# Performance work log

Hardware: AMD Instinct MI355X
Metric: run time of the kernel (lower is better)

## Reference

```python
import jax, jax.numpy as jnp
import numpy as np

EMB_DIM = 2048
N_Q_HEADS = 32
N_KV_HEADS = 8
HEAD_DIM = EMB_DIM // N_Q_HEADS  # 64
N_REP = N_Q_HEADS // N_KV_HEADS  # 4
ROPE_BASE = 10000.0


def setup_inputs() -> dict:
    key = jax.random.key(0)
    ks = jax.random.split(key, 9)
    B, T = 2, 2048
    kv_dim = HEAD_DIM * N_KV_HEADS
    s = 0.02
    return {
        "x":  jax.random.normal(ks[0], (B, T, EMB_DIM), jnp.float32),
        "Wq": jax.random.normal(ks[1], (EMB_DIM, EMB_DIM), jnp.float32) * s,
        "bq": jax.random.normal(ks[2], (EMB_DIM,), jnp.float32) * s,
        "Wk": jax.random.normal(ks[3], (kv_dim, EMB_DIM), jnp.float32) * s,
        "bk": jax.random.normal(ks[4], (kv_dim,), jnp.float32) * s,
        "Wv": jax.random.normal(ks[5], (kv_dim, EMB_DIM), jnp.float32) * s,
        "bv": jax.random.normal(ks[6], (kv_dim,), jnp.float32) * s,
        "Wo": jax.random.normal(ks[7], (EMB_DIM, EMB_DIM), jnp.float32) * s,
        "bo": jax.random.normal(ks[8], (EMB_DIM,), jnp.float32) * s,
    }


def _rope_tables(T, D, dtype):
    inv_freq = 1.0 / (ROPE_BASE ** (jnp.arange(0, D, 2, dtype=jnp.float32) / D))
    t = jnp.arange(T, dtype=jnp.float32)
    freqs = jnp.einsum("i,j->ij", t, inv_freq)          # [T, D/2]
    emb = jnp.concatenate([freqs, freqs], axis=-1)       # [T, D]
    # broadcast over batch and heads: [1, T, 1, D]
    return jnp.cos(emb)[None, :, None, :].astype(dtype), jnp.sin(emb)[None, :, None, :].astype(dtype)


def _rotate_half(x):
    x1, x2 = jnp.split(x, 2, axis=-1)
    return jnp.concatenate([-x2, x1], axis=-1)


def reference(x, Wq, bq, Wk, bk, Wv, bv, Wo, bo):
    B, T, C = x.shape
    q = (x @ Wq.T + bq).reshape(B, T, N_Q_HEADS, HEAD_DIM)
    k = (x @ Wk.T + bk).reshape(B, T, N_KV_HEADS, HEAD_DIM)
    v = (x @ Wv.T + bv).reshape(B, T, N_KV_HEADS, HEAD_DIM)

    cos, sin = _rope_tables(T, HEAD_DIM, x.dtype)
    q = q * cos + _rotate_half(q) * sin
    k = k * cos + _rotate_half(k) * sin

    q = q.transpose(0, 2, 1, 3)                          # [B, Hq, T, D]
    k = k.transpose(0, 2, 1, 3)                          # [B, Hkv, T, D]
    v = v.transpose(0, 2, 1, 3)
    # GQA: repeat_interleave kv heads to match query heads
    k = jnp.repeat(k, N_REP, axis=1)                     # [B, Hq, T, D]
    v = jnp.repeat(v, N_REP, axis=1)

    scale = 1.0 / jnp.sqrt(jnp.asarray(HEAD_DIM, x.dtype))
    att = jnp.einsum("bhqd,bhkd->bhqk", q, k) * scale    # [B, Hq, T, T]
    causal = jnp.tril(jnp.ones((T, T), dtype=bool))
    att = jnp.where(causal[None, None], att, -jnp.inf)
    att = jax.nn.softmax(att, axis=-1)

    y = jnp.einsum("bhqk,bhkd->bhqd", att, v)            # [B, Hq, T, D]
    y = y.transpose(0, 2, 1, 3).reshape(B, T, C)
    return y @ Wo.T + bo
```

## Files before the change

kernel.cpp:

```cpp
#include <hip/hip_runtime.h>
#include <hip/hip_bf16.h>
#include <math.h>


typedef __attribute__((ext_vector_type(8))) short short8;
typedef __attribute__((ext_vector_type(4))) float f32x4;
typedef __attribute__((ext_vector_type(16))) float f32x16;
typedef __attribute__((ext_vector_type(2))) unsigned int uint2v;

#define MFMA16(a,b,c) __builtin_amdgcn_mfma_f32_16x16x32_bf16((a),(b),(c),0,0,0)
#define MFMA32(a,b,c) __builtin_amdgcn_mfma_f32_32x32x16_bf16((a),(b),(c),0,0,0)
#define QSCALE 0.18033688011112043f
#define NFREQ  (-13.28771237954945f / 32.0f)

__device__ __forceinline__ ushort f2bf(float f) {
  union { float f; unsigned u; } x; x.f = f;
  unsigned r = x.u + 0x7fffu + ((x.u >> 16) & 1u);
  return (ushort)(r >> 16);
}
__device__ __forceinline__ uint pkbf(float a, float b) {
  union { float f; unsigned u; } x, y; x.f = a; y.f = b;
  return ((x.u + 0x8000u) >> 16) | ((y.u + 0x8000u) & 0xffff0000u);
}

__device__ __forceinline__ void g2l16(const void* g, void* l) {
  __builtin_amdgcn_global_load_lds(
      (__attribute__((address_space(1))) void*)g,
      (__attribute__((address_space(3))) void*)l, 16, 0, 0);
}

__global__ void cvt_all(const float* __restrict__ x,  const float* __restrict__ wq,
                        const float* __restrict__ wk, const float* __restrict__ wv,
                        const float* __restrict__ wo,
                        ushort* __restrict__ x_bf, ushort* __restrict__ wqkv,
                        ushort* __restrict__ wo_bf) {
  int i = blockIdx.x * 256 + threadIdx.x;
  const float4* src; ushort* dst; int off;
  if (i < 2097152)      { src = (const float4*)x;  dst = x_bf;             off = i; }
  else if (i < 3145728) { src = (const float4*)wq; dst = wqkv;             off = i - 2097152; }
  else if (i < 3407872) { src = (const float4*)wk; dst = wqkv + 4194304;   off = i - 3145728; }
  else if (i < 3670016) { src = (const float4*)wv; dst = wqkv + 5242880;   off = i - 3407872; }
  else                  { src = (const float4*)wo; dst = wo_bf;            off = i - 3670016; }
  float4 v = src[off];
  ushort4 o;
  o.x = f2bf(v.x); o.y = f2bf(v.y); o.z = f2bf(v.z); o.w = f2bf(v.w);
  ((ushort4*)dst)[off] = o;
}

__global__ __launch_bounds__(256, 3)
void gemm_qkv(const ushort* __restrict__ A, const ushort* __restrict__ Bw,
              const float* __restrict__ bq, const float* __restrict__ bk,
              const float* __restrict__ bv,
              ushort* __restrict__ qr, ushort* __restrict__ kr,
              ushort* __restrict__ vt) {
  const int K = 2048;
  __shared__ ushort As[2][128*32];
  __shared__ ushort Bs[2][128*32];
  const int tid = threadIdx.x;
  const int wave = tid >> 6, lane = tid & 63;
  const int wm = wave >> 1, wn = wave & 1;
  const int quad = lane >> 4, l16 = lane & 15;
  const int swg = (l16 >> 1) & 3;
  int id = blockIdx.y * 24 + blockIdx.x;
  id = (id & 7) * 96 + (id >> 3);
  const int bx = id % 24, by = id / 24;
  const int m0 = by * 128, n0 = bx * 128;

  f32x4 acc[4][4] = {};

  auto stage = [&](int buf, int k0) {
#pragma unroll
    for (int i = 0; i < 2; ++i) {
      int cbase = (i*4 + wave) * 64;
      int p = cbase + lane;
      int row = p >> 2, pcb = p & 3;
      int cl = pcb ^ ((row >> 1) & 3);
      g2l16(A  + (size_t)(m0 + row) * K + k0 + cl * 8, As[buf] + (size_t)cbase * 8);
      g2l16(Bw + (size_t)(n0 + row) * K + k0 + cl * 8, Bs[buf] + (size_t)cbase * 8);
    }
  };

  stage(0, 0);
  for (int k0 = 0; k0 < K; k0 += 32) {
    __syncthreads();
    int cur = (k0 >> 5) & 1;
    if (k0 + 32 < K) stage(cur ^ 1, k0 + 32);

    short8 af[4], bfr[4];
#pragma unroll
    for (int mi = 0; mi < 4; ++mi)
      af[mi] = *(const short8*)(As[cur] + (wm*64 + mi*16 + l16)*32 + ((quad ^ swg) * 8));
#pragma unroll
    for (int ni = 0; ni < 4; ++ni)
      bfr[ni] = *(const short8*)(Bs[cur] + (wn*64 + ni*16 + l16)*32 + ((quad ^ swg) * 8));
#pragma unroll
    for (int mi = 0; mi < 4; ++mi)
#pragma unroll
      for (int ni = 0; ni < 4; ++ni)
        acc[mi][ni] = MFMA16(af[mi], bfr[ni], acc[mi][ni]);
  }

  const int bb = m0 >> 11;
  const int tb = (m0 & 2047) + wm*64;

  if (bx < 20) {
    const bool isq = bx < 16;
    const float scale = isq ? QSCALE : 1.0f;
#pragma unroll
    for (int ni = 0; ni < 2; ++ni) {
      int n = n0 + wn*64 + ni*16 + l16;
      int d = ni*16 + l16;
      float bias1, bias2;
      ushort* dst;
      if (isq) {
        bias1 = bq[n]; bias2 = bq[n + 32];
        dst = qr + ((size_t)(bb*32 + (n >> 6)) * 2048) * 64 + d;
      } else {
        bias1 = bk[n - 2048]; bias2 = bk[n - 2016];
        dst = kr + ((size_t)(bb*8 + ((n >> 6) - 32)) * 2048) * 64 + d;
      }
      float invf = exp2f((float)d * NFREQ);
#pragma unroll
      for (int mi = 0; mi < 4; ++mi) {
#pragma unroll
        for (int r = 0; r < 4; ++r) {
          int t = tb + mi*16 + quad*4 + r;
          float x1 = acc[mi][ni][r]   + bias1;
          float x2 = acc[mi][ni+2][r] + bias2;
          float f = (float)t * invf;
          float sn = __sinf(f), cs = __cosf(f);
          dst[(size_t)t*64]      = f2bf((x1*cs - x2*sn) * scale);
          dst[(size_t)t*64 + 32] = f2bf((x2*cs + x1*sn) * scale);
        }
      }
    }
  } else {
#pragma unroll
    for (int ni = 0; ni < 4; ++ni) {
      int n = n0 + wn*64 + ni*16 + l16;
      int d = ni*16 + l16;
      float bias = bv[n - 2560];
      ushort* dst = vt + ((size_t)(bb*8 + ((n - 2560) >> 6)) * 64 + d) * 2048;
#pragma unroll
      for (int mi = 0; mi < 4; ++mi) {
        int t = tb + mi*16 + quad*4;
        uint2 pk;
        pk.x = (uint)f2bf(acc[mi][ni][0]+bias) | ((uint)f2bf(acc[mi][ni][1]+bias) << 16);
        pk.y = (uint)f2bf(acc[mi][ni][2]+bias) | ((uint)f2bf(acc[mi][ni][3]+bias) << 16);
        *(uint2*)(dst + t) = pk;
      }
    }
  }
}

__global__ __launch_bounds__(256, 3)
void gemm128(const ushort* __restrict__ A, const ushort* __restrict__ Bw,
             const float* __restrict__ b0,
             float* __restrict__ Cout, int M, int N, int K) {
  __shared__ ushort As[2][128*32];
  __shared__ ushort Bs[2][128*32];
  const int tid = threadIdx.x;
  const int wave = tid >> 6, lane = tid & 63;
  const int wm = wave >> 1, wn = wave & 1;
  const int quad = lane >> 4, l16 = lane & 15;
  const int swg = (l16 >> 1) & 3;
  int id = blockIdx.y * 16 + blockIdx.x;
  id = (id & 7) * 64 + (id >> 3);
  const int m0 = (id / 16) * 128, n0 = (id % 16) * 128;

  f32x4 acc[4][4] = {};

  auto stage = [&](int buf, int k0) {
#pragma unroll
    for (int i = 0; i < 2; ++i) {
      int cbase = (i*4 + wave) * 64;
      int p = cbase + lane;
      int row = p >> 2, pcb = p & 3;
      int cl = pcb ^ ((row >> 1) & 3);
      g2l16(A  + (size_t)(m0 + row) * K + k0 + cl * 8, As[buf] + (size_t)cbase * 8);
      g2l16(Bw + (size_t)(n0 + row) * K + k0 + cl * 8, Bs[buf] + (size_t)cbase * 8);
    }
  };

  stage(0, 0);
  for (int k0 = 0; k0 < K; k0 += 32) {
    __syncthreads();
    int cur = (k0 >> 5) & 1;
    if (k0 + 32 < K) stage(cur ^ 1, k0 + 32);

    short8 af[4], bfr[4];
#pragma unroll
    for (int mi = 0; mi < 4; ++mi)
      af[mi] = *(const short8*)(As[cur] + (wm*64 + mi*16 + l16)*32 + ((quad ^ swg) * 8));
#pragma unroll
    for (int ni = 0; ni < 4; ++ni)
      bfr[ni] = *(const short8*)(Bs[cur] + (wn*64 + ni*16 + l16)*32 + ((quad ^ swg) * 8));
#pragma unroll
    for (int mi = 0; mi < 4; ++mi)
#pragma unroll
      for (int ni = 0; ni < 4; ++ni)
        acc[mi][ni] = MFMA16(af[mi], bfr[ni], acc[mi][ni]);
  }

#pragma unroll
  for (int ni = 0; ni < 4; ++ni) {
    int n = n0 + wn*64 + ni*16 + l16;
    float bias = b0[n];
#pragma unroll
    for (int mi = 0; mi < 4; ++mi) {
#pragma unroll
      for (int r = 0; r < 4; ++r) {
        int m = m0 + wm*64 + mi*16 + quad*4 + r;
        Cout[(size_t)m * N + n] = acc[mi][ni][r] + bias;
      }
    }
  }
}

__global__ __launch_bounds__(256, 4)
void attn(const ushort* __restrict__ Q, const ushort* __restrict__ Kb,
          const ushort* __restrict__ Vt, ushort* __restrict__ Y) {
  __shared__ ushort Ks[2][64*64];
  __shared__ ushort Vs[2][64*64];
  const int tid = threadIdx.x, wave = tid >> 6, lane = tid & 63;
  const int l32 = lane & 31, hh = lane >> 5;
  const int h = blockIdx.y, b = blockIdx.z;
  const int hk = h >> 2;
  const ushort* Qb = Q  + ((size_t)(b*32 + h)  * 2048) * 64;
  const ushort* Kg = Kb + ((size_t)(b*8 + hk) * 2048) * 64;
  const ushort* Vg = Vt + ((size_t)(b*8 + hk) * 64) * 2048;

  auto stage = [&](int buf, int kt) {
#pragma unroll
    for (int i = 0; i < 2; ++i) {
      int p = i*256 + tid;
      int row = p >> 3, pcb = p & 7;
      int cl = pcb ^ (row & 7);
      g2l16(Kg + (size_t)(kt*64 + row)*64 + cl*8, Ks[buf] + (size_t)p*8);
      g2l16(Vg + (size_t)row*2048 + kt*64 + cl*8, Vs[buf] + (size_t)p*8);
    }
  };

  const int qt = (blockIdx.y & 16) ? (15 - blockIdx.x) : blockIdx.x;
  const int q0 = qt * 128;
  const int qrow = q0 + wave*32 + l32;
  short8 qf[4];
#pragma unroll
  for (int ks = 0; ks < 4; ++ks)
    qf[ks] = *(const short8*)(Qb + (size_t)qrow*64 + ks*16 + hh*8);

  f32x16 o[2] = {};
  float lsum = 0.f;

  stage(0, 0);

  const int ktmax = qt*2 + 1;
  for (int kt = 0; kt <= ktmax; ++kt) {
    __syncthreads();
    int cur = kt & 1;
    if (kt < ktmax) stage(cur ^ 1, kt + 1);

    const bool band = (kt*64 + 63 > q0 + wave*32);

#pragma unroll
    for (int kb = 0; kb < 2; ++kb) {
      f32x16 s = {};
      __builtin_amdgcn_s_setprio(1);
#pragma unroll
      for (int ks = 0; ks < 4; ++ks) {
        int row = kb*32 + l32;
        short8 kf = *(const short8*)(Ks[cur] + row*64 + (((ks*2 + hh) ^ (row & 7)) * 8));
        s = MFMA32(kf, qf[ks], s);
      }
      __builtin_amdgcn_s_setprio(0);

      if (band) {
#pragma unroll
        for (int r = 0; r < 16; ++r) {
          int key = kt*64 + kb*32 + (r & 3) + 8*(r >> 2) + 4*hh;
          if (key > qrow) s[r] = -INFINITY;
        }
      }

#pragma unroll
      for (int r = 0; r < 16; ++r) {
        s[r] = __builtin_amdgcn_exp2f(s[r]);
        lsum += s[r];
      }

      __builtin_amdgcn_s_setprio(1);
#pragma unroll
      for (int c = 0; c < 2; ++c) {
        int rb = c*8;
        uint a0 = pkbf(s[rb+0], s[rb+1]);
        uint b0 = pkbf(s[rb+4], s[rb+5]);
        uint a1 = pkbf(s[rb+2], s[rb+3]);
        uint b1 = pkbf(s[rb+6], s[rb+7]);
        uint2v r0 = __builtin_amdgcn_permlane32_swap(a0, b0, false, false);
        uint2v r1 = __builtin_amdgcn_permlane32_swap(a1, b1, false, false);
        union { uint u[4]; short8 s8; } pa;
        pa.u[0] = r0[0]; pa.u[1] = r1[0]; pa.u[2] = r0[1]; pa.u[3] = r1[1];
#pragma unroll
        for (int db = 0; db < 2; ++db) {
          int row = db*32 + l32;
          short8 vf = *(const short8*)(Vs[cur] + row*64 +
                        (((kb*4 + c*2 + hh) ^ (row & 7)) * 8));
          o[db] = MFMA32(vf, pa.s8, o[db]);
        }
      }
      __builtin_amdgcn_s_setprio(0);
    }
  }

  union { float f; uint u; } lu; lu.f = lsum;
  uint2v lr = __builtin_amdgcn_permlane32_swap(lu.u, lu.u, false, false);
  union { uint u; float f; } la, lb; la.u = lr[0]; lb.u = lr[1];
  float inv = 1.0f / (la.f + lb.f);

#pragma unroll
  for (int db = 0; db < 2; ++db) {
#pragma unroll
    for (int g = 0; g < 4; ++g) {
      int d = db*32 + 8*g + 4*hh;
      size_t base = ((size_t)(b*2048 + qrow)) * 2048 + h*64 + d;
      uint2 pk;
      pk.x = pkbf(o[db][4*g+0]*inv, o[db][4*g+1]*inv);
      pk.y = pkbf(o[db][4*g+2]*inv, o[db][4*g+3]*inv);
      *(uint2*)((ushort*)Y + base) = pk;
    }
  }
}

extern "C" void kernel_launch(void* const* d_in, const int* in_sizes, int n_in,
                              void* d_out, int out_size, void* d_ws, size_t ws_size,
                              hipStream_t stream) {
  (void)in_sizes; (void)n_in; (void)out_size; (void)ws_size;
  const float* x  = (const float*)d_in[0];
  const float* Wq = (const float*)d_in[1];
  const float* bq = (const float*)d_in[2];
  const float* Wk = (const float*)d_in[3];
  const float* bk = (const float*)d_in[4];
  const float* Wv = (const float*)d_in[5];
  const float* bv = (const float*)d_in[6];
  const float* Wo = (const float*)d_in[7];
  const float* bo = (const float*)d_in[8];
  float* out = (float*)d_out;

  ushort* ws    = (ushort*)d_ws;
  ushort* x_bf  = ws;
  ushort* wqkv  = x_bf + 8388608;
  ushort* wo_bf = wqkv + 6291456;
  ushort* qr    = wo_bf + 4194304;
  ushort* kr    = qr + 8388608;
  ushort* vt    = kr + 2097152;
  ushort* Y     = x_bf;

  cvt_all<<<18432, 256, 0, stream>>>(x, Wq, Wk, Wv, Wo, x_bf, wqkv, wo_bf);
  gemm_qkv<<<dim3(24, 32), 256, 0, stream>>>(x_bf, wqkv, bq, bk, bv, qr, kr, vt);
  attn<<<dim3(16, 32, 2), 256, 0, stream>>>(qr, kr, vt, Y);
  gemm128<<<dim3(16, 32), 256, 0, stream>>>(Y, wo_bf, bo, out, 4096, 2048, 2048);
}
```

Baseline: 294.4 us.

## Drop LDS staging in attention, read K/V from global, pair causal tiles per block

The attention kernel no longer stages K and V tiles into double-buffered shared memory with barriers. Each wave now loads its MFMA fragments straight from global memory and relies on the caches. Each block processes two complementary query tiles (qt and 15-qt) in sequence to balance the causal work, and the grid is halved. Block indices are also remapped so that blocks sharing a KV head are spread across XCDs. This removes LDS traffic and barriers, but each wave now makes redundant uncoalesced global loads, especially the strided V reads.

```diff
diff --git a/kernel.cpp b/kernel.cpp
--- a/kernel.cpp
+++ b/kernel.cpp
@@ -217,116 +217,100 @@
   }
 }
 
-__global__ __launch_bounds__(256, 4)
+__global__ __launch_bounds__(256, 2)
 void attn(const ushort* __restrict__ Q, const ushort* __restrict__ Kb,
           const ushort* __restrict__ Vt, ushort* __restrict__ Y) {
-  __shared__ ushort Ks[2][64*64];
-  __shared__ ushort Vs[2][64*64];
   const int tid = threadIdx.x, wave = tid >> 6, lane = tid & 63;
   const int l32 = lane & 31, hh = lane >> 5;
-  const int h = blockIdx.y, b = blockIdx.z;
+  int lin = blockIdx.z * 256 + blockIdx.y * 8 + blockIdx.x;
+  int wid = (lin & 7) * 64 + (lin >> 3);
+  const int xq = wid & 7;
+  const int h = (wid >> 3) & 31, b = wid >> 8;
   const int hk = h >> 2;
   const ushort* Qb = Q  + ((size_t)(b*32 + h)  * 2048) * 64;
   const ushort* Kg = Kb + ((size_t)(b*8 + hk) * 2048) * 64;
   const ushort* Vg = Vt + ((size_t)(b*8 + hk) * 64) * 2048;
 
-  auto stage = [&](int buf, int kt) {
-#pragma unroll
-    for (int i = 0; i < 2; ++i) {
-      int p = i*256 + tid;
-      int row = p >> 3, pcb = p & 7;
-      int cl = pcb ^ (row & 7);
-      g2l16(Kg + (size_t)(kt*64 + row)*64 + cl*8, Ks[buf] + (size_t)p*8);
-      g2l16(Vg + (size_t)row*2048 + kt*64 + cl*8, Vs[buf] + (size_t)p*8);
-    }
-  };
-
-  const int qt = (blockIdx.y & 16) ? (15 - blockIdx.x) : blockIdx.x;
-  const int q0 = qt * 128;
-  const int qrow = q0 + wave*32 + l32;
-  short8 qf[4];
-#pragma unroll
-  for (int ks = 0; ks < 4; ++ks)
-    qf[ks] = *(const short8*)(Qb + (size_t)qrow*64 + ks*16 + hh*8);
-
-  f32x16 o[2] = {};
-  float lsum = 0.f;
-
-  stage(0, 0);
-
-  const int ktmax = qt*2 + 1;
-  for (int kt = 0; kt <= ktmax; ++kt) {
-    __syncthreads();
-    int cur = kt & 1;
-    if (kt < ktmax) stage(cur ^ 1, kt + 1);
-
-    const bool band = (kt*64 + 63 > q0 + wave*32);
-
-#pragma unroll
-    for (int kb = 0; kb < 2; ++kb) {
-      f32x16 s = {};
-      __builtin_amdgcn_s_setprio(1);
-#pragma unroll
-      for (int ks = 0; ks < 4; ++ks) {
-        int row = kb*32 + l32;
-        short8 kf = *(const short8*)(Ks[cur] + row*64 + (((ks*2 + hh) ^ (row & 7)) * 8));
-        s = MFMA32(kf, qf[ks], s);
-      }
-      __builtin_amdgcn_s_setprio(0);
-
-      if (band) {
+  for (int pass = 0; pass < 2; ++pass) {
+    const int qt = pass ? (15 - xq) : xq;
+    const int q0 = qt * 128;
+    const int qrow = q0 + wave*32 + l32;
+    short8 qf[4];
+#pragma unroll
+    for (int ks = 0; ks < 4; ++ks)
+      qf[ks] = *(const short8*)(Qb + (size_t)qrow*64 + ks*16 + hh*8);
+
+    f32x16 o[2] = {};
+    float lsum = 0.f;
+
+    const int ktmax = qt*2 + 1;
+    for (int kt = 0; kt <= ktmax; ++kt) {
+      const bool band = (kt*64 + 63 > q0 + wave*32);
+
+#pragma unroll
+      for (int kb = 0; kb < 2; ++kb) {
+        f32x16 s = {};
+        __builtin_amdgcn_s_setprio(1);
+#pragma unroll
+        for (int ks = 0; ks < 4; ++ks) {
+          short8 kf = *(const short8*)(Kg + (size_t)(kt*64 + kb*32 + l32)*64 + ks*16 + hh*8);
+          s = MFMA32(kf, qf[ks], s);
+        }
+        __builtin_amdgcn_s_setprio(0);
+
+        if (band) {
+#pragma unroll
+          for (int r = 0; r < 16; ++r) {
+            int key = kt*64 + kb*32 + (r & 3) + 8*(r >> 2) + 4*hh;
+            if (key > qrow) s[r] = -INFINITY;
+          }
+        }
+
 #pragma unroll
         for (int r = 0; r < 16; ++r) {
-          int key = kt*64 + kb*32 + (r & 3) + 8*(r >> 2) + 4*hh;
-          if (key > qrow) s[r] = -INFINITY;
-        }
-      }
-
-#pragma unroll
-      for (int r = 0; r < 16; ++r) {
-        s[r] = __builtin_amdgcn_exp2f(s[r]);
-        lsum += s[r];
-      }
-
-      __builtin_amdgcn_s_setprio(1);
-#pragma unroll
-      for (int c = 0; c < 2; ++c) {
-        int rb = c*8;
-        uint a0 = pkbf(s[rb+0], s[rb+1]);
-        uint b0 = pkbf(s[rb+4], s[rb+5]);
-        uint a1 = pkbf(s[rb+2], s[rb+3]);
-        uint b1 = pkbf(s[rb+6], s[rb+7]);
-        uint2v r0 = __builtin_amdgcn_permlane32_swap(a0, b0, false, false);
-        uint2v r1 = __builtin_amdgcn_permlane32_swap(a1, b1, false, false);
-        union { uint u[4]; short8 s8; } pa;
-        pa.u[0] = r0[0]; pa.u[1] = r1[0]; pa.u[2] = r0[1]; pa.u[3] = r1[1];
-#pragma unroll
-        for (int db = 0; db < 2; ++db) {
-          int row = db*32 + l32;
-          short8 vf = *(const short8*)(Vs[cur] + row*64 +
-                        (((kb*4 + c*2 + hh) ^ (row & 7)) * 8));
-          o[db] = MFMA32(vf, pa.s8, o[db]);
-        }
-      }
-      __builtin_amdgcn_s_setprio(0);
-    }
-  }
-
-  union { float f; uint u; } lu; lu.f = lsum;
-  uint2v lr = __builtin_amdgcn_permlane32_swap(lu.u, lu.u, false, false);
-  union { uint u; float f; } la, lb; la.u = lr[0]; lb.u = lr[1];
-  float inv = 1.0f / (la.f + lb.f);
-
-#pragma unroll
-  for (int db = 0; db < 2; ++db) {
-#pragma unroll
-    for (int g = 0; g < 4; ++g) {
-      int d = db*32 + 8*g + 4*hh;
-      size_t base = ((size_t)(b*2048 + qrow)) * 2048 + h*64 + d;
-      uint2 pk;
-      pk.x = pkbf(o[db][4*g+0]*inv, o[db][4*g+1]*inv);
-      pk.y = pkbf(o[db][4*g+2]*inv, o[db][4*g+3]*inv);
-      *(uint2*)((ushort*)Y + base) = pk;
+          s[r] = __builtin_amdgcn_exp2f(s[r]);
+          lsum += s[r];
+        }
+
+        __builtin_amdgcn_s_setprio(1);
+#pragma unroll
+        for (int c = 0; c < 2; ++c) {
+          int rb = c*8;
+          uint a0 = pkbf(s[rb+0], s[rb+1]);
+          uint b0 = pkbf(s[rb+4], s[rb+5]);
+          uint a1 = pkbf(s[rb+2], s[rb+3]);
+          uint b1 = pkbf(s[rb+6], s[rb+7]);
+          uint2v r0 = __builtin_amdgcn_permlane32_swap(a0, b0, false, false);
+          uint2v r1 = __builtin_amdgcn_permlane32_swap(a1, b1, false, false);
+          union { uint u[4]; short8 s8; } pa;
+          pa.u[0] = r0[0]; pa.u[1] = r1[0]; pa.u[2] = r0[1]; pa.u[3] = r1[1];
+#pragma unroll
+          for (int db = 0; db < 2; ++db) {
+            short8 vf = *(const short8*)(Vg + (size_t)(db*32 + l32)*2048
+                                            + kt*64 + (kb*4 + c*2 + hh)*8);
+            o[db] = MFMA32(vf, pa.s8, o[db]);
+          }
+        }
+        __builtin_amdgcn_s_setprio(0);
+      }
+    }
+
+    union { float f; uint u; } lu; lu.f = lsum;
+    uint2v lr = __builtin_amdgcn_permlane32_swap(lu.u, lu.u, false, false);
+    union { uint u; float f; } la, lb; la.u = lr[0]; lb.u = lr[1];
+    float inv = 1.0f / (la.f + lb.f);
+
+#pragma unroll
+    for (int db = 0; db < 2; ++db) {
+#pragma unroll
+      for (int g = 0; g < 4; ++g) {
+        int d = db*32 + 8*g + 4*hh;
+        size_t base = ((size_t)(b*2048 + qrow)) * 2048 + h*64 + d;
+        uint2 pk;
+        pk.x = pkbf(o[db][4*g+0]*inv, o[db][4*g+1]*inv);
+        pk.y = pkbf(o[db][4*g+2]*inv, o[db][4*g+3]*inv);
+        *(uint2*)((ushort*)Y + base) = pk;
+      }
     }
   }
 }
@@ -357,6 +341,6 @@
 
   cvt_all<<<18432, 256, 0, stream>>>(x, Wq, Wk, Wv, Wo, x_bf, wqkv, wo_bf);
   gemm_qkv<<<dim3(24, 32), 256, 0, stream>>>(x_bf, wqkv, bq, bk, bv, qr, kr, vt);
-  attn<<<dim3(16, 32, 2), 256, 0, stream>>>(qr, kr, vt, Y);
+  attn<<<dim3(8, 32, 2), 256, 0, stream>>>(qr, kr, vt, Y);
   gemm128<<<dim3(16, 32), 256, 0, stream>>>(Y, wo_bf, bo, out, 4096, 2048, 2048);
 }
```

Measured after the change: 364.1 us. +23.7%, slower.

## Split attention KV loop across two wave groups and pair causal tiles per block

Applied to the files above, without the earlier changes.

The attention kernel now launches 512-thread blocks where two groups of four waves each process alternating KV tiles for the same query tile, then combine partial outputs and row sums through shared memory. Each block also handles two query tiles (qt and 15-qt) in sequence to balance causal work, halving the grid. This is meant to shorten the serial KV loop per query tile and balance load. In exchange it adds a shared-memory reduction, extra barriers, doubled LDS use and fewer blocks, which may lower occupancy.

```diff
diff --git a/kernel.cpp b/kernel.cpp
--- a/kernel.cpp
+++ b/kernel.cpp
@@ -217,12 +217,14 @@
   }
 }
 
-__global__ __launch_bounds__(256, 4)
+__global__ __launch_bounds__(512, 4)
 void attn(const ushort* __restrict__ Q, const ushort* __restrict__ Kb,
           const ushort* __restrict__ Vt, ushort* __restrict__ Y) {
-  __shared__ ushort Ks[2][64*64];
-  __shared__ ushort Vs[2][64*64];
+  __shared__ ushort Ks[2][2][64*64];
+  __shared__ ushort Vs[2][2][64*64];
   const int tid = threadIdx.x, wave = tid >> 6, lane = tid & 63;
+  const int wq = wave & 3;
+  const int par = wave >> 2;
   const int l32 = lane & 31, hh = lane >> 5;
   const int h = blockIdx.y, b = blockIdx.z;
   const int hk = h >> 2;
@@ -231,102 +233,137 @@
   const ushort* Vg = Vt + ((size_t)(b*8 + hk) * 64) * 2048;
 
   auto stage = [&](int buf, int kt) {
+    int qtid = wq*64 + lane;
 #pragma unroll
     for (int i = 0; i < 2; ++i) {
-      int p = i*256 + tid;
+      int p = i*256 + qtid;
       int row = p >> 3, pcb = p & 7;
       int cl = pcb ^ (row & 7);
-      g2l16(Kg + (size_t)(kt*64 + row)*64 + cl*8, Ks[buf] + (size_t)p*8);
-      g2l16(Vg + (size_t)row*2048 + kt*64 + cl*8, Vs[buf] + (size_t)p*8);
+      g2l16(Kg + (size_t)(kt*64 + row)*64 + cl*8, Ks[par][buf] + (size_t)p*8);
+      g2l16(Vg + (size_t)row*2048 + kt*64 + cl*8, Vs[par][buf] + (size_t)p*8);
     }
   };
 
-  const int qt = (blockIdx.y & 16) ? (15 - blockIdx.x) : blockIdx.x;
-  const int q0 = qt * 128;
-  const int qrow = q0 + wave*32 + l32;
-  short8 qf[4];
-#pragma unroll
-  for (int ks = 0; ks < 4; ++ks)
-    qf[ks] = *(const short8*)(Qb + (size_t)qrow*64 + ks*16 + hh*8);
-
-  f32x16 o[2] = {};
-  float lsum = 0.f;
-
-  stage(0, 0);
-
-  const int ktmax = qt*2 + 1;
-  for (int kt = 0; kt <= ktmax; ++kt) {
-    __syncthreads();
-    int cur = kt & 1;
-    if (kt < ktmax) stage(cur ^ 1, kt + 1);
-
-    const bool band = (kt*64 + 63 > q0 + wave*32);
-
-#pragma unroll
-    for (int kb = 0; kb < 2; ++kb) {
-      f32x16 s = {};
-      __builtin_amdgcn_s_setprio(1);
-#pragma unroll
-      for (int ks = 0; ks < 4; ++ks) {
-        int row = kb*32 + l32;
-        short8 kf = *(const short8*)(Ks[cur] + row*64 + (((ks*2 + hh) ^ (row & 7)) * 8));
-        s = MFMA32(kf, qf[ks], s);
-      }
-      __builtin_amdgcn_s_setprio(0);
-
-      if (band) {
+  for (int pass = 0; pass < 2; ++pass) {
+    const int qt = pass ? (15 - blockIdx.x) : blockIdx.x;
+    const int q0 = qt * 128;
+    const int qrow = q0 + wq*32 + l32;
+    short8 qf[4];
+#pragma unroll
+    for (int ks = 0; ks < 4; ++ks)
+      qf[ks] = *(const short8*)(Qb + (size_t)qrow*64 + ks*16 + hh*8);
+
+    f32x16 o[2] = {};
+    float lsum = 0.f;
+
+    __syncthreads();
+    const int nt = qt + 1;
+    stage(0, par);
+
+    for (int it = 0; it < nt; ++it) {
+      const int kt = par + it*2;
+      __syncthreads();
+      int cur = it & 1;
+      if (it + 1 < nt) stage(cur ^ 1, kt + 2);
+
+      const ushort* Kl = Ks[par][cur];
+      const ushort* Vl = Vs[par][cur];
+      const bool band = (kt*64 + 63 > q0 + wq*32);
+
+#pragma unroll
+      for (int kb = 0; kb < 2; ++kb) {
+        f32x16 s = {};
+        __builtin_amdgcn_s_setprio(1);
+#pragma unroll
+        for (int ks = 0; ks < 4; ++ks) {
+          int row = kb*32 + l32;
+          short8 kf = *(const short8*)(Kl + row*64 + (((ks*2 + hh) ^ (row & 7)) * 8));
+          s = MFMA32(kf, qf[ks], s);
+        }
+        __builtin_amdgcn_s_setprio(0);
+
+        if (band) {
+#pragma unroll
+          for (int r = 0; r < 16; ++r) {
+            int key = kt*64 + kb*32 + (r & 3) + 8*(r >> 2) + 4*hh;
+            if (key > qrow) s[r] = -INFINITY;
+          }
+        }
+
 #pragma unroll
         for (int r = 0; r < 16; ++r) {
-          int key = kt*64 + kb*32 + (r & 3) + 8*(r >> 2) + 4*hh;
-          if (key > qrow) s[r] = -INFINITY;
-        }
-      }
-
-#pragma unroll
-      for (int r = 0; r < 16; ++r) {
-        s[r] = __builtin_amdgcn_exp2f(s[r]);
-        lsum += s[r];
-      }
-
-      __builtin_amdgcn_s_setprio(1);
-#pragma unroll
-      for (int c = 0; c < 2; ++c) {
-        int rb = c*8;
-        uint a0 = pkbf(s[rb+0], s[rb+1]);
-        uint b0 = pkbf(s[rb+4], s[rb+5]);
-        uint a1 = pkbf(s[rb+2], s[rb+3]);
-        uint b1 = pkbf(s[rb+6], s[rb+7]);
-        uint2v r0 = __builtin_amdgcn_permlane32_swap(a0, b0, false, false);
-        uint2v r1 = __builtin_amdgcn_permlane32_swap(a1, b1, false, false);
-        union { uint u[4]; short8 s8; } pa;
-        pa.u[0] = r0[0]; pa.u[1] = r1[0]; pa.u[2] = r0[1]; pa.u[3] = r1[1];
-#pragma unroll
-        for (int db = 0; db < 2; ++db) {
-          int row = db*32 + l32;
-          short8 vf = *(const short8*)(Vs[cur] + row*64 +
-                        (((kb*4 + c*2 + hh) ^ (row & 7)) * 8));
-          o[db] = MFMA32(vf, pa.s8, o[db]);
-        }
-      }
-      __builtin_amdgcn_s_setprio(0);
-    }
-  }
-
-  union { float f; uint u; } lu; lu.f = lsum;
-  uint2v lr = __builtin_amdgcn_permlane32_swap(lu.u, lu.u, false, false);
-  union { uint u; float f; } la, lb; la.u = lr[0]; lb.u = lr[1];
-  float inv = 1.0f / (la.f + lb.f);
-
-#pragma unroll
-  for (int db = 0; db < 2; ++db) {
-#pragma unroll
-    for (int g = 0; g < 4; ++g) {
-      int d = db*32 + 8*g + 4*hh;
-      size_t base = ((size_t)(b*2048 + qrow)) * 2048 + h*64 + d;
-      uint2 pk;
-      pk.x = pkbf(o[db][4*g+0]*inv, o[db][4*g+1]*inv);
-      pk.y = pkbf(o[db][4*g+2]*inv, o[db][4*g+3]*inv);
-      *(uint2*)((ushort*)Y + base) = pk;
+          s[r] = __builtin_amdgcn_exp2f(s[r]);
+          lsum += s[r];
+        }
+
+        __builtin_amdgcn_s_setprio(1);
+#pragma unroll
+        for (int c = 0; c < 2; ++c) {
+          int rb = c*8;
+          uint a0 = pkbf(s[rb+0], s[rb+1]);
+          uint b0 = pkbf(s[rb+4], s[rb+5]);
+          uint a1 = pkbf(s[rb+2], s[rb+3]);
+          uint b1 = pkbf(s[rb+6], s[rb+7]);
+          uint2v r0 = __builtin_amdgcn_permlane32_swap(a0, b0, false, false);
+          uint2v r1 = __builtin_amdgcn_permlane32_swap(a1, b1, false, false);
+          union { uint u[4]; short8 s8; } pa;
+          pa.u[0] = r0[0]; pa.u[1] = r1[0]; pa.u[2] = r0[1]; pa.u[3] = r1[1];
+#pragma unroll
+          for (int db = 0; db < 2; ++db) {
+            int row = db*32 + l32;
+            short8 vf = *(const short8*)(Vl + row*64 +
+                          (((kb*4 + c*2 + hh) ^ (row & 7)) * 8));
+            o[db] = MFMA32(vf, pa.s8, o[db]);
+          }
+        }
+        __builtin_amdgcn_s_setprio(0);
+      }
+    }
+
+    __syncthreads();
+    float* ex  = (float*)&Ks[0][0][0];
+    float* exl = (float*)&Vs[0][0][0];
+    const int basei = (wq*64 + lane) * 32;
+    if (par == 1) {
+#pragma unroll
+      for (int db = 0; db < 2; ++db)
+#pragma unroll
+        for (int j = 0; j < 4; ++j) {
+          int cc = db*4 + j;
+          f32x4 v = { o[db][4*j+0], o[db][4*j+1], o[db][4*j+2], o[db][4*j+3] };
+          *(f32x4*)&ex[basei + ((cc ^ (lane & 7)) << 2)] = v;
+        }
+      exl[wq*64 + lane] = lsum;
+    }
+    __syncthreads();
+    if (par == 0) {
+#pragma unroll
+      for (int db = 0; db < 2; ++db)
+#pragma unroll
+        for (int j = 0; j < 4; ++j) {
+          int cc = db*4 + j;
+          f32x4 v = *(const f32x4*)&ex[basei + ((cc ^ (lane & 7)) << 2)];
+          o[db][4*j+0] += v[0]; o[db][4*j+1] += v[1];
+          o[db][4*j+2] += v[2]; o[db][4*j+3] += v[3];
+        }
+      lsum += exl[wq*64 + lane];
+
+      union { float f; uint u; } lu; lu.f = lsum;
+      uint2v lr = __builtin_amdgcn_permlane32_swap(lu.u, lu.u, false, false);
+      union { uint u; float f; } la, lb2; la.u = lr[0]; lb2.u = lr[1];
+      float inv = 1.0f / (la.f + lb2.f);
+
+#pragma unroll
+      for (int db = 0; db < 2; ++db)
+#pragma unroll
+        for (int g = 0; g < 4; ++g) {
+          int d = db*32 + 8*g + 4*hh;
+          size_t base = ((size_t)(b*2048 + qrow)) * 2048 + h*64 + d;
+          uint2 pk;
+          pk.x = pkbf(o[db][4*g+0]*inv, o[db][4*g+1]*inv);
+          pk.y = pkbf(o[db][4*g+2]*inv, o[db][4*g+3]*inv);
+          *(uint2*)((ushort*)Y + base) = pk;
+        }
     }
   }
 }
@@ -357,6 +394,6 @@
 
   cvt_all<<<18432, 256, 0, stream>>>(x, Wq, Wk, Wv, Wo, x_bf, wqkv, wo_bf);
   gemm_qkv<<<dim3(24, 32), 256, 0, stream>>>(x_bf, wqkv, bq, bk, bv, qr, kr, vt);
-  attn<<<dim3(16, 32, 2), 256, 0, stream>>>(qr, kr, vt, Y);
+  attn<<<dim3(8, 32, 2), 512, 0, stream>>>(qr, kr, vt, Y);
   gemm128<<<dim3(16, 32), 256, 0, stream>>>(Y, wo_bf, bo, out, 4096, 2048, 2048);
 }
```

Result: no change. 298.5 us (+1.4%).

## Use 128-key tiles and pair complementary query tiles per attention block

Applied to the files above, without the earlier changes.

The attention kernel now stages 128-key K/V tiles (doubling LDS buffers, with an adjusted V swizzle) and has each block process two complementary query tiles (qt and 15-qt) in sequence, halving the grid. This balances causal work per block and cuts barrier and stage overhead per key. On the diagonal tile, waves skip key sub-blocks that are fully masked. The costs are larger LDS use, a lower launch-bound occupancy target, and only 512 blocks, so fewer waves are available to hide latency.

```diff
diff --git a/kernel.cpp b/kernel.cpp
--- a/kernel.cpp
+++ b/kernel.cpp
@@ -217,11 +217,11 @@
   }
 }
 
-__global__ __launch_bounds__(256, 4)
+__global__ __launch_bounds__(256, 2)
 void attn(const ushort* __restrict__ Q, const ushort* __restrict__ Kb,
           const ushort* __restrict__ Vt, ushort* __restrict__ Y) {
-  __shared__ ushort Ks[2][64*64];
-  __shared__ ushort Vs[2][64*64];
+  __shared__ ushort Ks[2][128*64];
+  __shared__ ushort Vs[2][64*128];
   const int tid = threadIdx.x, wave = tid >> 6, lane = tid & 63;
   const int l32 = lane & 31, hh = lane >> 5;
   const int h = blockIdx.y, b = blockIdx.z;
@@ -232,101 +232,109 @@
 
   auto stage = [&](int buf, int kt) {
 #pragma unroll
-    for (int i = 0; i < 2; ++i) {
+    for (int i = 0; i < 4; ++i) {
       int p = i*256 + tid;
-      int row = p >> 3, pcb = p & 7;
-      int cl = pcb ^ (row & 7);
-      g2l16(Kg + (size_t)(kt*64 + row)*64 + cl*8, Ks[buf] + (size_t)p*8);
-      g2l16(Vg + (size_t)row*2048 + kt*64 + cl*8, Vs[buf] + (size_t)p*8);
+      int krow = p >> 3, kcb = p & 7;
+      int kcl = kcb ^ (krow & 7);
+      g2l16(Kg + (size_t)(kt*128 + krow)*64 + kcl*8, Ks[buf] + (size_t)p*8);
+      int vrow = p >> 4, vcb = p & 15;
+      int vcl = vcb ^ (vrow & 15);
+      g2l16(Vg + (size_t)vrow*2048 + kt*128 + vcl*8, Vs[buf] + (size_t)p*8);
     }
   };
 
-  const int qt = (blockIdx.y & 16) ? (15 - blockIdx.x) : blockIdx.x;
-  const int q0 = qt * 128;
-  const int qrow = q0 + wave*32 + l32;
-  short8 qf[4];
-#pragma unroll
-  for (int ks = 0; ks < 4; ++ks)
-    qf[ks] = *(const short8*)(Qb + (size_t)qrow*64 + ks*16 + hh*8);
-
-  f32x16 o[2] = {};
-  float lsum = 0.f;
-
-  stage(0, 0);
-
-  const int ktmax = qt*2 + 1;
-  for (int kt = 0; kt <= ktmax; ++kt) {
+  for (int pass = 0; pass < 2; ++pass) {
+    const int qt = pass ? (15 - blockIdx.x) : blockIdx.x;
+    const int q0 = qt * 128;
+    const int qrow = q0 + wave*32 + l32;
+    short8 qf[4];
+#pragma unroll
+    for (int ks = 0; ks < 4; ++ks)
+      qf[ks] = *(const short8*)(Qb + (size_t)qrow*64 + ks*16 + hh*8);
+
+    f32x16 o[2] = {};
+    float lsum = 0.f;
+
     __syncthreads();
-    int cur = kt & 1;
-    if (kt < ktmax) stage(cur ^ 1, kt + 1);
-
-    const bool band = (kt*64 + 63 > q0 + wave*32);
-
-#pragma unroll
-    for (int kb = 0; kb < 2; ++kb) {
-      f32x16 s = {};
-      __builtin_amdgcn_s_setprio(1);
-#pragma unroll
-      for (int ks = 0; ks < 4; ++ks) {
-        int row = kb*32 + l32;
-        short8 kf = *(const short8*)(Ks[cur] + row*64 + (((ks*2 + hh) ^ (row & 7)) * 8));
-        s = MFMA32(kf, qf[ks], s);
-      }
-      __builtin_amdgcn_s_setprio(0);
-
-      if (band) {
+    stage(0, 0);
+
+    for (int kt = 0; kt <= qt; ++kt) {
+      __syncthreads();
+      int cur = kt & 1;
+      if (kt < qt) stage(cur ^ 1, kt + 1);
+
+      const ushort* Kl = Ks[cur];
+      const ushort* Vl = Vs[cur];
+      const bool diag = (kt == qt);
+
+#pragma unroll
+      for (int kb = 0; kb < 4; ++kb) {
+        if (diag && kb > wave) continue;
+
+        f32x16 s = {};
+        __builtin_amdgcn_s_setprio(1);
+#pragma unroll
+        for (int ks = 0; ks < 4; ++ks) {
+          int row = kb*32 + l32;
+          short8 kf = *(const short8*)(Kl + row*64 + (((ks*2 + hh) ^ (row & 7)) * 8));
+          s = MFMA32(kf, qf[ks], s);
+        }
+        __builtin_amdgcn_s_setprio(0);
+
+        if (diag && kb == wave) {
+#pragma unroll
+          for (int r = 0; r < 16; ++r) {
+            int key = kt*128 + kb*32 + (r & 3) + 8*(r >> 2) + 4*hh;
+            if (key > qrow) s[r] = -INFINITY;
+          }
+        }
+
 #pragma unroll
         for (int r = 0; r < 16; ++r) {
-          int key = kt*64 + kb*32 + (r & 3) + 8*(r >> 2) + 4*hh;
-          if (key > qrow) s[r] = -INFINITY;
-        }
-      }
-
-#pragma unroll
-      for (int r = 0; r < 16; ++r) {
-        s[r] = __builtin_amdgcn_exp2f(s[r]);
-        lsum += s[r];
-      }
-
-      __builtin_amdgcn_s_setprio(1);
-#pragma unroll
-      for (int c = 0; c < 2; ++c) {
-        int rb = c*8;
-        uint a0 = pkbf(s[rb+0], s[rb+1]);
-        uint b0 = pkbf(s[rb+4], s[rb+5]);
-        uint a1 = pkbf(s[rb+2], s[rb+3]);
-        uint b1 = pkbf(s[rb+6], s[rb+7]);
-        uint2v r0 = __builtin_amdgcn_permlane32_swap(a0, b0, false, false);
-        uint2v r1 = __builtin_amdgcn_permlane32_swap(a1, b1, false, false);
-        union { uint u[4]; short8 s8; } pa;
-        pa.u[0] = r0[0]; pa.u[1] = r1[0]; pa.u[2] = r0[1]; pa.u[3] = r1[1];
-#pragma unroll
-        for (int db = 0; db < 2; ++db) {
-          int row = db*32 + l32;
-          short8 vf = *(const short8*)(Vs[cur] + row*64 +
-                        (((kb*4 + c*2 + hh) ^ (row & 7)) * 8));
-          o[db] = MFMA32(vf, pa.s8, o[db]);
-        }
-      }
-      __builtin_amdgcn_s_setprio(0);
-    }
-  }
-
-  union { float f; uint u; } lu; lu.f = lsum;
-  uint2v lr = __builtin_amdgcn_permlane32_swap(lu.u, lu.u, false, false);
-  union { uint u; float f; } la, lb; la.u = lr[0]; lb.u = lr[1];
-  float inv = 1.0f / (la.f + lb.f);
-
-#pragma unroll
-  for (int db = 0; db < 2; ++db) {
-#pragma unroll
-    for (int g = 0; g < 4; ++g) {
-      int d = db*32 + 8*g + 4*hh;
-      size_t base = ((size_t)(b*2048 + qrow)) * 2048 + h*64 + d;
-      uint2 pk;
-      pk.x = pkbf(o[db][4*g+0]*inv, o[db][4*g+1]*inv);
-      pk.y = pkbf(o[db][4*g+2]*inv, o[db][4*g+3]*inv);
-      *(uint2*)((ushort*)Y + base) = pk;
+          s[r] = __builtin_amdgcn_exp2f(s[r]);
+          lsum += s[r];
+        }
+
+        __builtin_amdgcn_s_setprio(1);
+#pragma unroll
+        for (int c = 0; c < 2; ++c) {
+          int rb = c*8;
+          uint a0 = pkbf(s[rb+0], s[rb+1]);
+          uint b0 = pkbf(s[rb+4], s[rb+5]);
+          uint a1 = pkbf(s[rb+2], s[rb+3]);
+          uint b1 = pkbf(s[rb+6], s[rb+7]);
+          uint2v r0 = __builtin_amdgcn_permlane32_swap(a0, b0, false, false);
+          uint2v r1 = __builtin_amdgcn_permlane32_swap(a1, b1, false, false);
+          union { uint u[4]; short8 s8; } pa;
+          pa.u[0] = r0[0]; pa.u[1] = r1[0]; pa.u[2] = r0[1]; pa.u[3] = r1[1];
+#pragma unroll
+          for (int db = 0; db < 2; ++db) {
+            int row = db*32 + l32;
+            int w = kb*4 + c*2 + hh;
+            short8 vf = *(const short8*)(Vl + row*128 + ((w ^ (row & 15)) * 8));
+            o[db] = MFMA32(vf, pa.s8, o[db]);
+          }
+        }
+        __builtin_amdgcn_s_setprio(0);
+      }
+    }
+
+    union { float f; uint u; } lu; lu.f = lsum;
+    uint2v lr = __builtin_amdgcn_permlane32_swap(lu.u, lu.u, false, false);
+    union { uint u; float f; } la, lb; la.u = lr[0]; lb.u = lr[1];
+    float inv = 1.0f / (la.f + lb.f);
+
+#pragma unroll
+    for (int db = 0; db < 2; ++db) {
+#pragma unroll
+      for (int g = 0; g < 4; ++g) {
+        int d = db*32 + 8*g + 4*hh;
+        size_t base = ((size_t)(b*2048 + qrow)) * 2048 + h*64 + d;
+        uint2 pk;
+        pk.x = pkbf(o[db][4*g+0]*inv, o[db][4*g+1]*inv);
+        pk.y = pkbf(o[db][4*g+2]*inv, o[db][4*g+3]*inv);
+        *(uint2*)((ushort*)Y + base) = pk;
+      }
     }
   }
 }
@@ -357,6 +365,6 @@
 
   cvt_all<<<18432, 256, 0, stream>>>(x, Wq, Wk, Wv, Wo, x_bf, wqkv, wo_bf);
   gemm_qkv<<<dim3(24, 32), 256, 0, stream>>>(x_bf, wqkv, bq, bk, bv, qr, kr, vt);
-  attn<<<dim3(16, 32, 2), 256, 0, stream>>>(qr, kr, vt, Y);
+  attn<<<dim3(8, 32, 2), 256, 0, stream>>>(qr, kr, vt, Y);
   gemm128<<<dim3(16, 32), 256, 0, stream>>>(Y, wo_bf, bo, out, 4096, 2048, 2048);
 }
```

Result: faster. 283.7 us (-3.6%).
